# Kernel tuning notes

Hardware: AMD Instinct MI355X
Metric: run time of the kernel (lower is better)

## Reference

```python
import jax, jax.numpy as jnp
import numpy as np

B, IN, OUT = 4096, 512, 512
NUM_KNOTS, DEGREE = 10, 3


def setup_inputs() -> dict:
    key = jax.random.key(0)
    k1, k2 = jax.random.split(key)
    x = jax.random.normal(k1, (B, IN), dtype=jnp.float32)
    # coefficients of all out*in edge splines: [out, in, num_knots-1, degree+1]
    coeff = jax.random.normal(k2, (OUT, IN, NUM_KNOTS - 1, DEGREE + 1), dtype=jnp.float32) * 0.1
    scale = jnp.ones((OUT,), dtype=jnp.float32)
    return {"x": x, "coeff": coeff, "scale": scale}


def reference(x, coeff, scale):
    # x: [B, IN]; coeff: [OUT, IN, S, P]; scale: [OUT]
    out_f, in_f, S, P = coeff.shape
    K = S + 1
    knots = jnp.linspace(-1.0, 1.0, K)            # shared uniform knots
    xc = jnp.clip(x, -1.0, 1.0)
    seg = jnp.clip(jnp.searchsorted(knots[1:], xc), 0, S - 1)  # [B, IN]
    lo = knots[seg]
    t = (xc - lo) / (knots[seg + 1] - lo)          # [B, IN]
    tpow = t[..., None] ** jnp.arange(P, dtype=x.dtype)        # [B, IN, P]
    onehot = jax.nn.one_hot(seg, S, dtype=x.dtype)             # [B, IN, S]
    # A[b,i,s,p] = onehot * t^p ; contraction with coeff is a single GEMM
    A = onehot[..., :, None] * tpow[..., None, :]              # [B, IN, S, P]
    y = jnp.einsum('bisp,jisp->bj', A, coeff)                  # [B, OUT]
    return y * scale
```

## Files before the change

kernel.cpp:

```cpp
#include <hip/hip_runtime.h>

#define B_DIM   4096
#define IN_DIM  512
#define OUT_DIM 512
#define KTOT    18432
#define BK      32
#define KSPLIT  8
#define KPER    2304
#define NT      72

using f32x4 = __attribute__((ext_vector_type(4))) float;
using s16x8 = __attribute__((ext_vector_type(8))) short;
using u32x4 = __attribute__((ext_vector_type(4))) unsigned int;

__device__ __forceinline__ unsigned int f2bf(float f) {
    unsigned int u = __float_as_uint(f);
    return (u + 0x7FFFu + ((u >> 16) & 1u)) >> 16;
}

__device__ __forceinline__ void glds16(const void* g, void* l) {
    __builtin_amdgcn_global_load_lds(
        (const __attribute__((address_space(1))) unsigned int*)g,
        (__attribute__((address_space(3))) unsigned int*)l,
        16, 0, 0);
}

__device__ __forceinline__ uint2 spline_rec_packed(float xv) {
    float xc = fminf(fmaxf(xv, -1.0f), 1.0f);
    double xd = (double)xc;
    int s = 0;
#pragma unroll
    for (int k = 1; k <= 8; ++k)
        s += ((-1.0 + (double)k * (2.0 / 9.0)) < xd) ? 1 : 0;
    double lo = -1.0 + (double)s * (2.0 / 9.0);
    double hi = -1.0 + (double)(s + 1) * (2.0 / 9.0);
    float t  = (float)((xd - lo) / (hi - lo));
    float t2 = t * t, t3 = t2 * t;
    uint2 r;
    r.x = f2bf(t)  | (f2bf(t2) << 16);
    r.y = f2bf(t3) | ((unsigned int)s << 16);
    return r;
}

__global__ void prep_x_kernel(const float* __restrict__ x, uint2* __restrict__ tp) {
    int idx = blockIdx.x * 256 + threadIdx.x;
    if (idx >= B_DIM * IN_DIM) return;
    tp[idx] = spline_rec_packed(x[idx]);
}

__global__ void prep_coeff2(const float* __restrict__ c,
                            const float* __restrict__ scale,
                            u32x4* __restrict__ cbf2) {
    int g = blockIdx.x * 256 + threadIdx.x;
    if (g >= (OUT_DIM * KTOT) / 8) return;
    int row = g & 127;
    int oct = (g >> 7) & 3;
    int hi  = g >> 9;
    int ntg = hi / 576;
    int kt  = hi - ntg * 576;
    int j = ntg * 128 + row;
    int k = kt * 32 + oct * 8;
    float s = scale[j];
    const float* src = c + (size_t)j * KTOT + k;
    f32x4 a = *(const f32x4*)src;
    f32x4 b = *(const f32x4*)(src + 4);
    u32x4 o;
    o.x = f2bf(a.x * s) | (f2bf(a.y * s) << 16);
    o.y = f2bf(a.z * s) | (f2bf(a.w * s) << 16);
    o.z = f2bf(b.x * s) | (f2bf(b.y * s) << 16);
    o.w = f2bf(b.z * s) | (f2bf(b.w * s) << 16);
    cbf2[g] = o;
}

__device__ __forceinline__ void scat2(char* Aq, int ar, int ah,
                                      uint2 q0, uint2 q1, int ifirst, int k0) {
#pragma unroll
    for (int cc = 0; cc < 2; ++cc) {
        uint2 rec = cc == 0 ? q0 : q1;
        int i = ifirst + cc;
        if (i < IN_DIM) {
            int s = (int)(rec.y >> 16);
            int off = i * 36 + s * 4 - k0;
            if (off >= 0 && off < BK && ((off >> 4) == ah)) {
                uint2 w;
                w.x = 0x3F80u | (rec.x << 16);
                w.y = (rec.x >> 16) | (rec.y << 16);
                *(uint2*)(Aq + (off >> 3) * 2048 + ar * 16 + (off & 4) * 2) = w;
            }
        }
    }
}

__launch_bounds__(256, 4)
__global__ void kan_gemm_db(const unsigned short* __restrict__ cbf2,
                            const uint2* __restrict__ tp,
                            float* __restrict__ out) {
    __shared__ u32x4 ldsRaw[32768 / 16];
    char* lds = (char*)ldsRaw;

    const int tid  = threadIdx.x;
    const int lane = tid & 63;
    const int wave = tid >> 6;
    const int wm = wave >> 1, wn = wave & 1;
    const int l15 = lane & 15, lhi = lane >> 4;

    const int bid = blockIdx.x;
    const int nt = bid & 3;
    const int ks = (bid >> 2) & 7;
    const int mt = bid >> 5;
    const int m0g = mt * 128, n0g = nt * 128;
    const int kbase = ks * KPER;

    const int ar = tid & 127, ah = tid >> 7;

    const uint2* tpRow = tp + (size_t)(m0g + ar) * IN_DIM;
    const char*  cbase = (const char*)cbf2 + (size_t)(nt * 576 + ks * NT) * 8192;

    f32x4 acc[4][4] = {};
    uint2 r0, r1;

    {
        char* A0 = lds;
        char* B0 = lds + 16384;
#pragma unroll
        for (int it = 0; it < 2; ++it)
            glds16(cbase + it * 4096 + tid * 16, B0 + it * 4096 + tid * 16);
        const int if0 = kbase / 36;
        uint2 q0 = tpRow[if0];
        uint2 q1 = tpRow[if0 + 1 < IN_DIM ? if0 + 1 : IN_DIM - 1];
        u32x4 z = {};
#pragma unroll
        for (int zi = 0; zi < 2; ++zi)
            *(u32x4*)(A0 + (ah * 2 + zi) * 2048 + ar * 16) = z;
        scat2(A0, ar, ah, q0, q1, if0, kbase);
        const int if1 = (kbase + BK) / 36;
        r0 = tpRow[if1];
        r1 = tpRow[if1 + 1 < IN_DIM ? if1 + 1 : IN_DIM - 1];
        __syncthreads();
    }

    for (int t = 0; t < NT; ++t) {
        const int p = t & 1;
        const char* Ap = lds + p * 8192;
        const char* Bp = lds + 16384 + p * 8192;
        char* Aq = lds + (p ^ 1) * 8192;
        char* Bq = lds + 16384 + (p ^ 1) * 8192;

        if (t + 1 < NT) {
            const int k0n = kbase + (t + 1) * BK;
            const char* srcT = cbase + (size_t)(t + 1) * 8192;
#pragma unroll
            for (int it = 0; it < 2; ++it)
                glds16(srcT + it * 4096 + tid * 16, Bq + it * 4096 + tid * 16);
            u32x4 z = {};
#pragma unroll
            for (int zi = 0; zi < 2; ++zi)
                *(u32x4*)(Aq + (ah * 2 + zi) * 2048 + ar * 16) = z;
            scat2(Aq, ar, ah, r0, r1, k0n / 36, k0n);
            const int tn = t + 2 < NT ? t + 2 : NT - 1;
            const int ifn = (kbase + tn * BK) / 36;
            r0 = tpRow[ifn];
            r1 = tpRow[ifn + 1 < IN_DIM ? ifn + 1 : IN_DIM - 1];
        }

        {
            s16x8 a[4], b[4];
#pragma unroll
            for (int mf = 0; mf < 4; ++mf)
                a[mf] = *(const s16x8*)(Ap + lhi * 2048 + (wm * 64 + mf * 16 + l15) * 16);
#pragma unroll
            for (int nf = 0; nf < 4; ++nf)
                b[nf] = *(const s16x8*)(Bp + lhi * 2048 + (wn * 64 + nf * 16 + l15) * 16);
#pragma unroll
            for (int mf = 0; mf < 4; ++mf)
#pragma unroll
                for (int nf = 0; nf < 4; ++nf)
                    acc[mf][nf] = __builtin_amdgcn_mfma_f32_16x16x32_bf16(a[mf], b[nf], acc[mf][nf], 0, 0, 0);
        }

        __syncthreads();
    }

#pragma unroll
    for (int mf = 0; mf < 4; ++mf) {
        const int rg = m0g + wm * 64 + mf * 16 + lhi * 4;
#pragma unroll
        for (int nf = 0; nf < 4; ++nf) {
            const int cg = n0g + wn * 64 + nf * 16 + l15;
#pragma unroll
            for (int e = 0; e < 4; ++e)
                atomicAdd(out + (size_t)(rg + e) * OUT_DIM + cg, acc[mf][nf][e]);
        }
    }
}

#define BM 128
#define BN 128
#define FBK 64
#define FKPER  4608
#define FSTEPS 72
__launch_bounds__(256, 2)
__global__ void kan_gemm_ref(const float* __restrict__ x,
                             const float* __restrict__ coeff,
                             const float* __restrict__ scale,
                             float* __restrict__ out) {
    __shared__ unsigned short AsF[BM * 72];
    __shared__ unsigned short BsF[8 * BN * 8];
    const int tid  = threadIdx.x;
    const int lane = tid & 63;
    const int wave = tid >> 6;
    const int wm = wave >> 1, wn = wave & 1;
    const int l15 = lane & 15, lhi = lane >> 4;
    const int bid = blockIdx.x;
    const int nt = bid & 3;
    const int ks = (bid >> 2) & 3;
    const int mt = bid >> 4;
    const int m0g = mt * BM, n0g = nt * BN, kbase = ks * FKPER;
    const int ar = tid >> 1, ah = tid & 1;
    const int abrow = m0g + ar;
    const int bjg = n0g + (tid & 127);
    const float bscale = scale[bjg];
    char* AsB = (char*)AsF;
    char* BsB = (char*)BsF;
    f32x4 acc[4][4] = {};
    for (int step = 0; step < FSTEPS; ++step) {
        const int k0 = kbase + step * FBK;
        {
            char* rb = AsB + ar * 144;
            u32x4 z = {};
            if (ah == 0) {
#pragma unroll
                for (int z4 = 0; z4 < 4; ++z4) *(u32x4*)(rb + z4 * 16) = z;
            } else {
#pragma unroll
                for (int z4 = 4; z4 < 9; ++z4) *(u32x4*)(rb + z4 * 16) = z;
            }
            const int ifirst = k0 / 36;
#pragma unroll
            for (int ii = 0; ii < 2; ++ii) {
                const int cand = ah + ii * 2;
                const int i = ifirst + cand;
                if (cand < 3 && i * 36 < k0 + FBK && i < IN_DIM) {
                    uint2 rec = spline_rec_packed(x[(size_t)abrow * IN_DIM + i]);
                    int s = (int)(rec.y >> 16);
                    const int off = i * 36 + s * 4 - k0;
                    unsigned int w0 = 0x3F80u | (rec.x << 16);
                    unsigned int w1 = (rec.x >> 16) | (rec.y << 16);
                    if (off >= 0 && off <= 62) *(unsigned int*)(rb + off * 2) = w0;
                    const int off2 = off + 2;
                    if (off2 >= 0 && off2 <= 62) *(unsigned int*)(rb + off2 * 2) = w1;
                }
            }
        }
#pragma unroll
        for (int it = 0; it < 4; ++it) {
            const int q  = it * 256 + tid;
            const int c  = q >> 7;
            const int kk = k0 + c * 8;
            f32x4 a = *(const f32x4*)(coeff + (size_t)bjg * KTOT + kk);
            f32x4 b = *(const f32x4*)(coeff + (size_t)bjg * KTOT + kk + 4);
            u32x4 o;
            o.x = f2bf(a.x * bscale) | (f2bf(a.y * bscale) << 16);
            o.y = f2bf(a.z * bscale) | (f2bf(a.w * bscale) << 16);
            o.z = f2bf(b.x * bscale) | (f2bf(b.y * bscale) << 16);
            o.w = f2bf(b.z * bscale) | (f2bf(b.w * bscale) << 16);
            *(u32x4*)(BsB + q * 16) = o;
        }
        __syncthreads();
#pragma unroll
        for (int kh = 0; kh < 2; ++kh) {
            const int kk = kh * 32;
            s16x8 a[4], b[4];
#pragma unroll
            for (int mf = 0; mf < 4; ++mf)
                a[mf] = *(const s16x8*)(AsB + (wm * 64 + mf * 16 + l15) * 144 + (kk + lhi * 8) * 2);
#pragma unroll
            for (int nf = 0; nf < 4; ++nf)
                b[nf] = *(const s16x8*)(BsB + (kh * 4 + lhi) * 2048 + (wn * 64 + nf * 16 + l15) * 16);
#pragma unroll
            for (int mf = 0; mf < 4; ++mf)
#pragma unroll
                for (int nf = 0; nf < 4; ++nf)
                    acc[mf][nf] = __builtin_amdgcn_mfma_f32_16x16x32_bf16(a[mf], b[nf], acc[mf][nf], 0, 0, 0);
        }
        __syncthreads();
    }
#pragma unroll
    for (int mf = 0; mf < 4; ++mf) {
        const int cmBase = m0g + wm * 64 + mf * 16 + lhi * 4;
#pragma unroll
        for (int nf = 0; nf < 4; ++nf) {
            const int cn = n0g + wn * 64 + nf * 16 + l15;
#pragma unroll
            for (int e = 0; e < 4; ++e)
                atomicAdd(out + (size_t)(cmBase + e) * OUT_DIM + cn, acc[mf][nf][e]);
        }
    }
}

extern "C" void kernel_launch(void* const* d_in, const int* in_sizes, int n_in,
                              void* d_out, int out_size, void* d_ws, size_t ws_size,
                              hipStream_t stream) {
    const float* x     = (const float*)d_in[0];
    const float* coeff = (const float*)d_in[1];
    const float* scale = (const float*)d_in[2];
    float* out = (float*)d_out;

    const size_t SZ_CBF = (size_t)OUT_DIM * KTOT * 2;
    const size_t SZ_TP  = (size_t)B_DIM * IN_DIM * 8;
    const size_t NEED   = SZ_CBF + SZ_TP;

    hipMemsetAsync(d_out, 0, (size_t)B_DIM * OUT_DIM * sizeof(float), stream);

    if (ws_size >= NEED) {
        unsigned short* cbf2 = (unsigned short*)d_ws;
        uint2*          tp   = (uint2*)((char*)d_ws + SZ_CBF);
        prep_coeff2<<<4608, 256, 0, stream>>>(coeff, scale, (u32x4*)cbf2);
        prep_x_kernel<<<8192, 256, 0, stream>>>(x, tp);
        kan_gemm_db<<<1024, 256, 0, stream>>>(cbf2, tp, out);
    } else {
        kan_gemm_ref<<<512, 256, 0, stream>>>(x, coeff, scale, out);
    }
}
```

Before: 164.0 us.

## Use 256x128 tiles with 8 waves, triple-buffered B, and two-phase MFMA pipeline

The GEMM kernel moves to 512-thread blocks covering a 256-row M tile, which halves the block count and reuses each B tile across twice as many rows. B is now triple-buffered and prefetched two steps ahead with global_load_lds. Each K step is split into two phases that interleave the LDS A-scatter and fragment loads with MFMA groups, using raw barriers, sched_barrier and setprio in place of __syncthreads. The aim is to hide load and scatter latency behind the matrix ops. The cost is 56KB of LDS per block and a doubled thread count, which may limit occupancy, plus more barriers per K step.

```diff
diff --git a/kernel.cpp b/kernel.cpp
--- a/kernel.cpp
+++ b/kernel.cpp
@@ -72,8 +72,8 @@
     cbf2[g] = o;
 }
 
-__device__ __forceinline__ void scat2(char* Aq, int ar, int ah,
-                                      uint2 q0, uint2 q1, int ifirst, int k0) {
+__device__ __forceinline__ void scat2a(char* Aq, int ar, int ah,
+                                       uint2 q0, uint2 q1, int ifirst, int k0) {
 #pragma unroll
     for (int cc = 0; cc < 2; ++cc) {
         uint2 rec = cc == 0 ? q0 : q1;
@@ -85,17 +85,24 @@
                 uint2 w;
                 w.x = 0x3F80u | (rec.x << 16);
                 w.y = (rec.x >> 16) | (rec.y << 16);
-                *(uint2*)(Aq + (off >> 3) * 2048 + ar * 16 + (off & 4) * 2) = w;
+                *(uint2*)(Aq + (off >> 3) * 4096 + ar * 16 + (off & 4) * 2) = w;
             }
         }
     }
 }
 
-__launch_bounds__(256, 4)
-__global__ void kan_gemm_db(const unsigned short* __restrict__ cbf2,
-                            const uint2* __restrict__ tp,
-                            float* __restrict__ out) {
-    __shared__ u32x4 ldsRaw[32768 / 16];
+#define BAR()   __builtin_amdgcn_s_barrier()
+#define SB0()   __builtin_amdgcn_sched_barrier(0)
+#define WLGKM() asm volatile("s_waitcnt lgkmcnt(0)" ::: "memory")
+#define WVM0()  asm volatile("s_waitcnt vmcnt(0)"   ::: "memory")
+#define PHASE_MID() BAR(); WLGKM(); SB0(); __builtin_amdgcn_s_setprio(1)
+#define PHASE_END() __builtin_amdgcn_s_setprio(0); BAR()
+
+__launch_bounds__(512, 4)
+__global__ void kan_gemm9(const unsigned short* __restrict__ cbf2,
+                          const uint2* __restrict__ tp,
+                          float* __restrict__ out) {
+    __shared__ u32x4 ldsRaw[57344 / 16];
     char* lds = (char*)ldsRaw;
 
     const int tid  = threadIdx.x;
@@ -105,80 +112,93 @@
     const int l15 = lane & 15, lhi = lane >> 4;
 
     const int bid = blockIdx.x;
+    const int mt = bid >> 5;
+    const int ks = (bid >> 2) & 7;
     const int nt = bid & 3;
-    const int ks = (bid >> 2) & 7;
-    const int mt = bid >> 5;
-    const int m0g = mt * 128, n0g = nt * 128;
+    const int m0g = mt * 256, n0g = nt * 128;
     const int kbase = ks * KPER;
 
-    const int ar = tid & 127, ah = tid >> 7;
+    const int ar = tid & 255, ah = tid >> 8;
 
     const uint2* tpRow = tp + (size_t)(m0g + ar) * IN_DIM;
     const char*  cbase = (const char*)cbf2 + (size_t)(nt * 576 + ks * NT) * 8192;
 
+    const int aoff = (wm * 64 + l15) * 16;
+    const int boff = (wn * 64 + l15) * 16;
+
     f32x4 acc[4][4] = {};
+    s16x8 av[2], bv[4];
     uint2 r0, r1;
 
     {
         char* A0 = lds;
-        char* B0 = lds + 16384;
-#pragma unroll
-        for (int it = 0; it < 2; ++it)
-            glds16(cbase + it * 4096 + tid * 16, B0 + it * 4096 + tid * 16);
         const int if0 = kbase / 36;
         uint2 q0 = tpRow[if0];
         uint2 q1 = tpRow[if0 + 1 < IN_DIM ? if0 + 1 : IN_DIM - 1];
         u32x4 z = {};
-#pragma unroll
-        for (int zi = 0; zi < 2; ++zi)
-            *(u32x4*)(A0 + (ah * 2 + zi) * 2048 + ar * 16) = z;
-        scat2(A0, ar, ah, q0, q1, if0, kbase);
+        *(u32x4*)(A0 + (ah * 2 + 0) * 4096 + ar * 16) = z;
+        *(u32x4*)(A0 + (ah * 2 + 1) * 4096 + ar * 16) = z;
+        scat2a(A0, ar, ah, q0, q1, if0, kbase);
+        glds16(cbase + tid * 16,        lds + 32768 + tid * 16);
+        glds16(cbase + 8192 + tid * 16, lds + 40960 + tid * 16);
         const int if1 = (kbase + BK) / 36;
         r0 = tpRow[if1];
         r1 = tpRow[if1 + 1 < IN_DIM ? if1 + 1 : IN_DIM - 1];
-        __syncthreads();
-    }
-
+        WVM0();
+        WLGKM();
+        BAR();
+        SB0();
+    }
+
+    int bcur = 0, bstg = 2;
     for (int t = 0; t < NT; ++t) {
         const int p = t & 1;
-        const char* Ap = lds + p * 8192;
-        const char* Bp = lds + 16384 + p * 8192;
-        char* Aq = lds + (p ^ 1) * 8192;
-        char* Bq = lds + 16384 + (p ^ 1) * 8192;
-
-        if (t + 1 < NT) {
-            const int k0n = kbase + (t + 1) * BK;
-            const char* srcT = cbase + (size_t)(t + 1) * 8192;
-#pragma unroll
-            for (int it = 0; it < 2; ++it)
-                glds16(srcT + it * 4096 + tid * 16, Bq + it * 4096 + tid * 16);
-            u32x4 z = {};
-#pragma unroll
-            for (int zi = 0; zi < 2; ++zi)
-                *(u32x4*)(Aq + (ah * 2 + zi) * 2048 + ar * 16) = z;
-            scat2(Aq, ar, ah, r0, r1, k0n / 36, k0n);
-            const int tn = t + 2 < NT ? t + 2 : NT - 1;
-            const int ifn = (kbase + tn * BK) / 36;
-            r0 = tpRow[ifn];
-            r1 = tpRow[ifn + 1 < IN_DIM ? ifn + 1 : IN_DIM - 1];
-        }
-
+        const char* Ap = lds + p * 16384;
+        char* Aq = lds + (p ^ 1) * 16384;
+        const char* Bp = lds + 32768 + bcur * 8192;
+        char* Bs = lds + 32768 + bstg * 8192;
+        const int tt1 = t + 1 < NT ? t + 1 : NT - 1;
+        const int tt2 = t + 2 < NT ? t + 2 : NT - 1;
+        const int k0n = kbase + tt1 * BK;
+        const char* srcT = cbase + (size_t)tt2 * 8192;
+        u32x4 z = {};
+
+#pragma unroll
+        for (int nf = 0; nf < 4; ++nf)
+            bv[nf] = *(const s16x8*)(Bp + lhi * 2048 + boff + nf * 256);
+#pragma unroll
+        for (int c = 0; c < 2; ++c)
+            av[c] = *(const s16x8*)(Ap + lhi * 4096 + aoff + c * 256);
+        *(u32x4*)(Aq + (ah * 2 + 0) * 4096 + ar * 16) = z;
+        glds16(srcT + tid * 16, Bs + tid * 16);
+        PHASE_MID();
+#pragma unroll
+        for (int mf = 0; mf < 2; ++mf)
+#pragma unroll
+            for (int nf = 0; nf < 4; ++nf)
+                acc[mf][nf] = __builtin_amdgcn_mfma_f32_16x16x32_bf16(av[mf], bv[nf], acc[mf][nf], 0, 0, 0);
+        PHASE_END();
+
+#pragma unroll
+        for (int c = 0; c < 2; ++c)
+            av[c] = *(const s16x8*)(Ap + lhi * 4096 + aoff + (2 + c) * 256);
+        *(u32x4*)(Aq + (ah * 2 + 1) * 4096 + ar * 16) = z;
+        scat2a(Aq, ar, ah, r0, r1, k0n / 36, k0n);
         {
-            s16x8 a[4], b[4];
-#pragma unroll
-            for (int mf = 0; mf < 4; ++mf)
-                a[mf] = *(const s16x8*)(Ap + lhi * 2048 + (wm * 64 + mf * 16 + l15) * 16);
+            const int if2 = (kbase + tt2 * BK) / 36;
+            r0 = tpRow[if2];
+            r1 = tpRow[if2 + 1 < IN_DIM ? if2 + 1 : IN_DIM - 1];
+        }
+        PHASE_MID();
+#pragma unroll
+        for (int mf = 0; mf < 2; ++mf)
 #pragma unroll
             for (int nf = 0; nf < 4; ++nf)
-                b[nf] = *(const s16x8*)(Bp + lhi * 2048 + (wn * 64 + nf * 16 + l15) * 16);
-#pragma unroll
-            for (int mf = 0; mf < 4; ++mf)
-#pragma unroll
-                for (int nf = 0; nf < 4; ++nf)
-                    acc[mf][nf] = __builtin_amdgcn_mfma_f32_16x16x32_bf16(a[mf], b[nf], acc[mf][nf], 0, 0, 0);
-        }
-
-        __syncthreads();
+                acc[2 + mf][nf] = __builtin_amdgcn_mfma_f32_16x16x32_bf16(av[mf], bv[nf], acc[2 + mf][nf], 0, 0, 0);
+        PHASE_END();
+
+        bcur = bcur == 2 ? 0 : bcur + 1;
+        bstg = bstg == 2 ? 0 : bstg + 1;
     }
 
 #pragma unroll
@@ -317,7 +337,7 @@
         uint2*          tp   = (uint2*)((char*)d_ws + SZ_CBF);
         prep_coeff2<<<4608, 256, 0, stream>>>(coeff, scale, (u32x4*)cbf2);
         prep_x_kernel<<<8192, 256, 0, stream>>>(x, tp);
-        kan_gemm_db<<<1024, 256, 0, stream>>>(cbf2, tp, out);
+        kan_gemm9<<<512, 512, 0, stream>>>(cbf2, tp, out);
     } else {
         kan_gemm_ref<<<512, 256, 0, stream>>>(x, coeff, scale, out);
     }
```

Measured after the change: 170.8 us. +4.1%, slower.
